# Performance work log

Hardware: AMD Instinct MI355X
Metric: run time of the kernel (lower is better)

## Reference

```python
import jax, jax.numpy as jnp
import numpy as np

H = 256      # hidden_size (hardcoded by view([-1,1,256]) in the torch source)
V = 50257    # output_size / vocab
L = 50       # max_length


def gru_cell(x, h, w_ih, w_hh, b_ih, b_hh):
    """PyTorch GRUCell semantics. x, h: [H]; w_*: [3H, H]; b_*: [3H]."""
    gi = w_ih @ x + b_ih
    gh = w_hh @ h + b_hh
    gi_r, gi_z, gi_n = jnp.split(gi, 3)
    gh_r, gh_z, gh_n = jnp.split(gh, 3)
    r = jax.nn.sigmoid(gi_r + gh_r)
    z = jax.nn.sigmoid(gi_z + gh_z)
    n = jnp.tanh(gi_n + r * gh_n)
    return (1.0 - z) * n + z * h


def setup_inputs() -> dict:
    key = jax.random.key(0)
    ks = jax.random.split(key, 24)
    p = lambda k, shape: (0.02 * jax.random.normal(k, shape)).astype(jnp.float32)
    d = {}
    d["token"] = jax.random.randint(ks[0], (1,), 0, V)
    d["hidden"] = jax.random.normal(ks[1], (1, 1, H), dtype=jnp.float32)
    d["encoder_outputs"] = jax.random.normal(ks[2], (L, H), dtype=jnp.float32)
    d["emb"] = p(ks[3], (V, H))
    d["attn_W"] = p(ks[4], (L, 2 * H)); d["attn_b"] = jnp.zeros((L,), jnp.float32)
    d["comb_W"] = p(ks[5], (H, 2 * H)); d["comb_b"] = jnp.zeros((H,), jnp.float32)
    # bidirectional GRU: forward (f) and reverse (b) direction weights
    d["w_ih_f"] = p(ks[6], (3 * H, H)); d["w_hh_f"] = p(ks[7], (3 * H, H))
    d["b_ih_f"] = jnp.zeros((3 * H,), jnp.float32); d["b_hh_f"] = jnp.zeros((3 * H,), jnp.float32)
    d["w_ih_b"] = p(ks[8], (3 * H, H)); d["w_hh_b"] = p(ks[9], (3 * H, H))
    d["b_ih_b"] = jnp.zeros((3 * H,), jnp.float32); d["b_hh_b"] = jnp.zeros((3 * H,), jnp.float32)
    # second (unidirectional) GRU
    d["w_ih_g"] = p(ks[10], (3 * H, H)); d["w_hh_g"] = p(ks[11], (3 * H, H))
    d["b_ih_g"] = jnp.zeros((3 * H,), jnp.float32); d["b_hh_g"] = jnp.zeros((3 * H,), jnp.float32)
    d["out_W"] = p(ks[12], (V, H)); d["out_b"] = jnp.zeros((V,), jnp.float32)
    return d


def reference(token, hidden, encoder_outputs, emb, attn_W, attn_b, comb_W, comb_b,
              w_ih_f, w_hh_f, b_ih_f, b_hh_f, w_ih_b, w_hh_b, b_ih_b, b_hh_b,
              w_ih_g, w_hh_g, b_ih_g, b_hh_g, out_W, out_b):
    # dropout is treated as identity (eval mode)
    e = emb[token[0]]                       # [H] embedded token
    h0 = hidden[0, 0]                       # [H]
    # attention weights over encoder positions
    aw = jax.nn.softmax(jax.nn.relu(attn_W @ jnp.concatenate([e, h0]) + attn_b))  # [L]
    applied = aw @ encoder_outputs          # [H]
    x = jax.nn.relu(comb_W @ jnp.concatenate([e, applied]) + comb_b)              # [H]
    # bidirectional GRU, seq_len=1: both directions see the same step, init hidden = h0
    hf = gru_cell(x, h0, w_ih_f, w_hh_f, b_ih_f, b_hh_f)
    hb = gru_cell(x, h0, w_ih_b, w_hh_b, b_ih_b, b_hh_b)
    hm = 0.5 * (hf + hb)                    # torch.mean(bihidden, dim=0)
    # bioutput (1,1,512) viewed as (2,1,256) -> second GRU runs 2 steps
    h1 = gru_cell(hf, hm, w_ih_g, w_hh_g, b_ih_g, b_hh_g)
    h2 = gru_cell(hb, h1, w_ih_g, w_hh_g, b_ih_g, b_hh_g)
    logp = jax.nn.log_softmax(out_W @ h1 + out_b)  # output[0] = first timestep = h1
    return (logp[None, :], h2[None, None, :], aw[None, :])
```

## Files before the change

kernel.cpp:

```cpp
#include <hip/hip_runtime.h>
#include <math.h>

#define H 256
#define L 50
#define V 50257
#define LOGIT_BLKS 786

__device__ __forceinline__ float dot4(float4 a, float4 b) {
    return a.x * b.x + a.y * b.y + a.z * b.z + a.w * b.w;
}

__device__ __forceinline__ float wave_reduce_sum(float v) {
#pragma unroll
    for (int m = 32; m >= 1; m >>= 1) v += __shfl_xor(v, m, 64);
    return v;
}

__device__ __forceinline__ float wave_reduce_max(float v) {
#pragma unroll
    for (int m = 32; m >= 1; m >>= 1) v = fmaxf(v, __shfl_xor(v, m, 64));
    return v;
}

__device__ __forceinline__ float sigmoidf(float x) { return 1.0f / (1.0f + __expf(-x)); }

__device__ __forceinline__ void ms_push(float& m, float& s, float x) {
    float mn = fmaxf(m, x);
    s = s * __expf(m - mn) + __expf(x - mn);
    m = mn;
}
__device__ __forceinline__ void ms_merge(float& m, float& s, float om, float os) {
    float M = fmaxf(m, om);
    float a = (m == -INFINITY) ? 0.f : s * __expf(m - M);
    float c = (om == -INFINITY) ? 0.f : os * __expf(om - M);
    m = M; s = a + c;
}

__device__ __forceinline__ void gru_wave(
    int j, int lane, float4 xv, float4 hv, float hj,
    const float* __restrict__ w_ih, const float* __restrict__ w_hh,
    const float* __restrict__ b_ih, const float* __restrict__ b_hh,
    float* __restrict__ outp)
{
    float gi[3], gh[3];
#pragma unroll
    for (int k = 0; k < 3; ++k) {
        int row = k * H + j;
        const float4* wi4 = (const float4*)(w_ih + (size_t)row * H);
        const float4* wh4 = (const float4*)(w_hh + (size_t)row * H);
        gi[k] = wave_reduce_sum(dot4(wi4[lane], xv)) + b_ih[row];
        gh[k] = wave_reduce_sum(dot4(wh4[lane], hv)) + b_hh[row];
    }
    if (lane == 0) {
        float r = sigmoidf(gi[0] + gh[0]);
        float z = sigmoidf(gi[1] + gh[1]);
        float n = tanhf(gi[2] + r * gh[2]);
        outp[j] = (1.f - z) * n + z * hj;
    }
}

__global__ __launch_bounds__(256) void k_scores(
    const int* __restrict__ token, const float* __restrict__ hidden,
    const float* __restrict__ emb, const float* __restrict__ attn_W,
    const float* __restrict__ attn_b, float* __restrict__ ws_scores)
{
    __shared__ float s_vec[2 * H];
    int t = threadIdx.x, wid = t >> 6, lane = t & 63;
    int tok = token[0];
    s_vec[t] = emb[(size_t)tok * H + t];
    s_vec[H + t] = hidden[t];
    __syncthreads();
    int row = blockIdx.x * 4 + wid;
    if (row < L) {
        float acc = 0.f;
#pragma unroll
        for (int c = 0; c < 8; ++c)
            acc += attn_W[row * 2 * H + c * 64 + lane] * s_vec[c * 64 + lane];
        acc = wave_reduce_sum(acc);
        if (lane == 0) ws_scores[row] = fmaxf(acc + attn_b[row], 0.f);
    }
}

__global__ __launch_bounds__(256) void k_comb(
    const int* __restrict__ token, const float* __restrict__ emb,
    const float* __restrict__ enc, const float* __restrict__ comb_W,
    const float* __restrict__ comb_b, const float* __restrict__ ws_scores,
    float* __restrict__ ws_x, float* __restrict__ out_aw)
{
    __shared__ __align__(16) float s_cat[2 * H];
    __shared__ float s_aw[64];
    int t = threadIdx.x, wid = t >> 6, lane = t & 63;
    int tok = token[0];
    s_cat[t] = emb[(size_t)tok * H + t];
    if (t < 64) {
        float v = (t < L) ? ws_scores[t] : -INFINITY;
        float mx = wave_reduce_max(v);
        float e = (t < L) ? __expf(v - mx) : 0.f;
        float ssum = wave_reduce_sum(e);
        if (t < L) {
            float aw = e / ssum;
            s_aw[t] = aw;
            if (blockIdx.x == 0) out_aw[t] = aw;
        }
    }
    __syncthreads();
    float app = 0.f;
    for (int l = 0; l < L; ++l) app += s_aw[l] * enc[l * H + t];
    s_cat[H + t] = app;
    __syncthreads();
    int row = blockIdx.x * 4 + wid;
    const float4* c4 = (const float4*)s_cat;
    const float4* W4 = (const float4*)(comb_W + (size_t)row * 2 * H);
    float acc = dot4(W4[lane], c4[lane]) + dot4(W4[lane + 64], c4[lane + 64]);
    acc = wave_reduce_sum(acc);
    if (lane == 0) ws_x[row] = fmaxf(acc + comb_b[row], 0.f);
}

__global__ __launch_bounds__(256) void k_gru_fb(
    const float* __restrict__ ws_x, const float* __restrict__ hidden,
    const float* __restrict__ w_ih_f, const float* __restrict__ w_hh_f,
    const float* __restrict__ b_ih_f, const float* __restrict__ b_hh_f,
    const float* __restrict__ w_ih_b, const float* __restrict__ w_hh_b,
    const float* __restrict__ b_ih_b, const float* __restrict__ b_hh_b,
    float* __restrict__ ws_hf, float* __restrict__ ws_hb)
{
    int t = threadIdx.x, wid = t >> 6, lane = t & 63;
    int g = blockIdx.x * 4 + wid;
    int dir = g >> 8, j = g & 255;
    gru_wave(j, lane, ((const float4*)ws_x)[lane], ((const float4*)hidden)[lane],
             hidden[j],
             dir ? w_ih_b : w_ih_f, dir ? w_hh_b : w_hh_f,
             dir ? b_ih_b : b_ih_f, dir ? b_hh_b : b_hh_f,
             dir ? ws_hb : ws_hf);
}

__global__ __launch_bounds__(256) void k_gru(
    const float* __restrict__ xvec, const float* __restrict__ ha,
    const float* __restrict__ hb,
    const float* __restrict__ w_ih, const float* __restrict__ w_hh,
    const float* __restrict__ b_ih, const float* __restrict__ b_hh,
    float* __restrict__ outp)
{
    int t = threadIdx.x, wid = t >> 6, lane = t & 63;
    int j = blockIdx.x * 4 + wid;
    float4 xv = ((const float4*)xvec)[lane];
    float4 hv = ((const float4*)ha)[lane];
    float hj;
    if (hb) {
        float4 bv = ((const float4*)hb)[lane];
        hv = make_float4(0.5f * (hv.x + bv.x), 0.5f * (hv.y + bv.y),
                         0.5f * (hv.z + bv.z), 0.5f * (hv.w + bv.w));
        hj = 0.5f * (ha[j] + hb[j]);
    } else {
        hj = ha[j];
    }
    gru_wave(j, lane, xv, hv, hj, w_ih, w_hh, b_ih, b_hh, outp);
}

__global__ __launch_bounds__(256) void k_logits(
    const float* __restrict__ out_W, const float* __restrict__ out_b,
    const float* __restrict__ h1, float* __restrict__ logits,
    float* __restrict__ part_m, float* __restrict__ part_s)
{
    __shared__ float s_m4[4], s_s4[4];
    int t = threadIdx.x, wid = t >> 6, lane = t & 63;
    float4 hv = ((const float4*)h1)[lane];
    int base = (blockIdx.x * 4 + wid) * 16;
    float m = -INFINITY, s = 0.f;
#pragma unroll 1
    for (int k = 0; k < 16; k += 2) {
        int v = base + k;
        if (v >= V) break;
        const float4* W0 = (const float4*)(out_W + (size_t)v * H);
        float4 a0 = W0[lane];
        bool has2 = (v + 1 < V);
        float4 a1 = has2 ? ((const float4*)(out_W + (size_t)(v + 1) * H))[lane]
                         : make_float4(0.f, 0.f, 0.f, 0.f);
        float x0 = wave_reduce_sum(dot4(a0, hv)) + out_b[v];
        float x1 = wave_reduce_sum(dot4(a1, hv));
        if (lane == 0) logits[v] = x0;
        ms_push(m, s, x0);
        if (has2) {
            x1 += out_b[v + 1];
            if (lane == 0) logits[v + 1] = x1;
            ms_push(m, s, x1);
        }
    }
    if (lane == 0) { s_m4[wid] = m; s_s4[wid] = s; }
    __syncthreads();
    if (t == 0) {
        float M = s_m4[0], S = s_s4[0];
#pragma unroll
        for (int q = 1; q < 4; ++q) ms_merge(M, S, s_m4[q], s_s4[q]);
        part_m[blockIdx.x] = M; part_s[blockIdx.x] = S;
    }
}

__global__ __launch_bounds__(256) void k_final(
    const float* __restrict__ part_m, const float* __restrict__ part_s,
    float* __restrict__ logits)
{
    __shared__ float s_m4[4], s_s4[4];
    __shared__ float s_bcast;
    int t = threadIdx.x, wid = t >> 6, lane = t & 63;
    float m = -INFINITY, s = 0.f;
    for (int idx = t; idx < LOGIT_BLKS; idx += 256)
        ms_merge(m, s, part_m[idx], part_s[idx]);
#pragma unroll
    for (int d = 32; d >= 1; d >>= 1) {
        float om = __shfl_xor(m, d, 64);
        float os = __shfl_xor(s, d, 64);
        ms_merge(m, s, om, os);
    }
    if (lane == 0) { s_m4[wid] = m; s_s4[wid] = s; }
    __syncthreads();
    if (t == 0) {
        float M = s_m4[0], S = s_s4[0];
#pragma unroll
        for (int q = 1; q < 4; ++q) ms_merge(M, S, s_m4[q], s_s4[q]);
        s_bcast = M + logf(S);
    }
    __syncthreads();
    float lse = s_bcast;
    int i = blockIdx.x * 256 + t;
    if (i < V) logits[i] -= lse;
}

extern "C" void kernel_launch(void* const* d_in, const int* in_sizes, int n_in,
                              void* d_out, int out_size, void* d_ws, size_t ws_size,
                              hipStream_t stream)
{
    const int*   token  = (const int*)d_in[0];
    const float* hidden = (const float*)d_in[1];
    const float* enc    = (const float*)d_in[2];
    const float* emb    = (const float*)d_in[3];
    const float* attn_W = (const float*)d_in[4];
    const float* attn_b = (const float*)d_in[5];
    const float* comb_W = (const float*)d_in[6];
    const float* comb_b = (const float*)d_in[7];
    const float* w_ih_f = (const float*)d_in[8];
    const float* w_hh_f = (const float*)d_in[9];
    const float* b_ih_f = (const float*)d_in[10];
    const float* b_hh_f = (const float*)d_in[11];
    const float* w_ih_b = (const float*)d_in[12];
    const float* w_hh_b = (const float*)d_in[13];
    const float* b_ih_b = (const float*)d_in[14];
    const float* b_hh_b = (const float*)d_in[15];
    const float* w_ih_g = (const float*)d_in[16];
    const float* w_hh_g = (const float*)d_in[17];
    const float* b_ih_g = (const float*)d_in[18];
    const float* b_hh_g = (const float*)d_in[19];
    const float* out_W  = (const float*)d_in[20];
    const float* out_b  = (const float*)d_in[21];

    float* out = (float*)d_out;
    float* ws  = (float*)d_ws;
    float* ws_scores = ws;
    float* ws_x      = ws + 64;
    float* ws_hf     = ws + 320;
    float* ws_hb     = ws + 576;
    float* ws_h1     = ws + 832;
    float* part_m    = ws + 1088;
    float* part_s    = ws + 1888;

    k_scores<<<13, 256, 0, stream>>>(token, hidden, emb, attn_W, attn_b, ws_scores);
    k_comb<<<64, 256, 0, stream>>>(token, emb, enc, comb_W, comb_b, ws_scores,
                                   ws_x, out + V + H);
    k_gru_fb<<<128, 256, 0, stream>>>(ws_x, hidden,
                                      w_ih_f, w_hh_f, b_ih_f, b_hh_f,
                                      w_ih_b, w_hh_b, b_ih_b, b_hh_b,
                                      ws_hf, ws_hb);
    k_gru<<<64, 256, 0, stream>>>(ws_hf, ws_hf, ws_hb,
                                  w_ih_g, w_hh_g, b_ih_g, b_hh_g, ws_h1);
    k_gru<<<64, 256, 0, stream>>>(ws_hb, ws_h1, nullptr,
                                  w_ih_g, w_hh_g, b_ih_g, b_hh_g, out + V);
    k_logits<<<LOGIT_BLKS, 256, 0, stream>>>(out_W, out_b, ws_h1, out,
                                             part_m, part_s);
    k_final<<<197, 256, 0, stream>>>(part_m, part_s, out);
}
```

Baseline: 179.0 us.

## Fuse attention scores into comb and second GRU step into logits kernel

Attention score computation moves into k_comb, so every block recomputes the 50 scores redundantly instead of running a separate launch. The second GRU step (h2) no longer gets its own launch; it runs as extra blocks inside the logits kernel, since neither depends on the other. The logits grid shrinks to 512 blocks with 25 rows per wave, which still covers V. Together these remove two kernel launches at the price of redundant attention work in each comb block.

```diff
diff --git a/kernel.cpp b/kernel.cpp
--- a/kernel.cpp
+++ b/kernel.cpp
@@ -4,7 +4,9 @@
 #define H 256
 #define L 50
 #define V 50257
-#define LOGIT_BLKS 786
+#define LOGIT_BLKS 512
+#define ROWS_PER_WAVE 25
+#define GRU2_BLKS 64
 
 __device__ __forceinline__ float dot4(float4 a, float4 b) {
     return a.x * b.x + a.y * b.y + a.z * b.z + a.w * b.w;
@@ -59,32 +61,11 @@
     }
 }
 
-__global__ __launch_bounds__(256) void k_scores(
+__global__ __launch_bounds__(256) void k_comb(
     const int* __restrict__ token, const float* __restrict__ hidden,
     const float* __restrict__ emb, const float* __restrict__ attn_W,
-    const float* __restrict__ attn_b, float* __restrict__ ws_scores)
-{
-    __shared__ float s_vec[2 * H];
-    int t = threadIdx.x, wid = t >> 6, lane = t & 63;
-    int tok = token[0];
-    s_vec[t] = emb[(size_t)tok * H + t];
-    s_vec[H + t] = hidden[t];
-    __syncthreads();
-    int row = blockIdx.x * 4 + wid;
-    if (row < L) {
-        float acc = 0.f;
-#pragma unroll
-        for (int c = 0; c < 8; ++c)
-            acc += attn_W[row * 2 * H + c * 64 + lane] * s_vec[c * 64 + lane];
-        acc = wave_reduce_sum(acc);
-        if (lane == 0) ws_scores[row] = fmaxf(acc + attn_b[row], 0.f);
-    }
-}
-
-__global__ __launch_bounds__(256) void k_comb(
-    const int* __restrict__ token, const float* __restrict__ emb,
-    const float* __restrict__ enc, const float* __restrict__ comb_W,
-    const float* __restrict__ comb_b, const float* __restrict__ ws_scores,
+    const float* __restrict__ attn_b, const float* __restrict__ enc,
+    const float* __restrict__ comb_W, const float* __restrict__ comb_b,
     float* __restrict__ ws_x, float* __restrict__ out_aw)
 {
     __shared__ __align__(16) float s_cat[2 * H];
@@ -92,8 +73,20 @@
     int t = threadIdx.x, wid = t >> 6, lane = t & 63;
     int tok = token[0];
     s_cat[t] = emb[(size_t)tok * H + t];
+    s_cat[H + t] = hidden[t];
+    __syncthreads();
+    const float4* c4 = (const float4*)s_cat;
+    float4 cA = c4[lane];
+    float4 cB = c4[lane + 64];
+    for (int r = wid; r < L; r += 4) {
+        const float4* W4 = (const float4*)(attn_W + (size_t)r * 2 * H);
+        float acc = dot4(W4[lane], cA) + dot4(W4[lane + 64], cB);
+        acc = wave_reduce_sum(acc);
+        if (lane == 0) s_aw[r] = fmaxf(acc + attn_b[r], 0.f);
+    }
+    __syncthreads();
     if (t < 64) {
-        float v = (t < L) ? ws_scores[t] : -INFINITY;
+        float v = (t < L) ? s_aw[t] : -INFINITY;
         float mx = wave_reduce_max(v);
         float e = (t < L) ? __expf(v - mx) : 0.f;
         float ssum = wave_reduce_sum(e);
@@ -109,9 +102,9 @@
     s_cat[H + t] = app;
     __syncthreads();
     int row = blockIdx.x * 4 + wid;
-    const float4* c4 = (const float4*)s_cat;
-    const float4* W4 = (const float4*)(comb_W + (size_t)row * 2 * H);
-    float acc = dot4(W4[lane], c4[lane]) + dot4(W4[lane + 64], c4[lane + 64]);
+    const float4* Wc = (const float4*)(comb_W + (size_t)row * 2 * H);
+    float4 cB2 = c4[lane + 64];
+    float acc = dot4(Wc[lane], cA) + dot4(Wc[lane + 64], cB2);
     acc = wave_reduce_sum(acc);
     if (lane == 0) ws_x[row] = fmaxf(acc + comb_b[row], 0.f);
 }
@@ -159,21 +152,31 @@
 
 __global__ __launch_bounds__(256) void k_logits(
     const float* __restrict__ out_W, const float* __restrict__ out_b,
-    const float* __restrict__ h1, float* __restrict__ logits,
-    float* __restrict__ part_m, float* __restrict__ part_s)
-{
+    const float* __restrict__ h1, const float* __restrict__ hb,
+    const float* __restrict__ w_ih_g, const float* __restrict__ w_hh_g,
+    const float* __restrict__ b_ih_g, const float* __restrict__ b_hh_g,
+    float* __restrict__ out_h2,
+    float* __restrict__ logits, float* __restrict__ part_m,
+    float* __restrict__ part_s)
+{
+    int t = threadIdx.x, wid = t >> 6, lane = t & 63;
+    if (blockIdx.x >= LOGIT_BLKS) {
+        int j = (blockIdx.x - LOGIT_BLKS) * 4 + wid;
+        gru_wave(j, lane, ((const float4*)hb)[lane], ((const float4*)h1)[lane],
+                 h1[j], w_ih_g, w_hh_g, b_ih_g, b_hh_g, out_h2);
+        return;
+    }
     __shared__ float s_m4[4], s_s4[4];
-    int t = threadIdx.x, wid = t >> 6, lane = t & 63;
     float4 hv = ((const float4*)h1)[lane];
-    int base = (blockIdx.x * 4 + wid) * 16;
+    int base = (blockIdx.x * 4 + wid) * ROWS_PER_WAVE;
     float m = -INFINITY, s = 0.f;
 #pragma unroll 1
-    for (int k = 0; k < 16; k += 2) {
+    for (int k = 0; k < ROWS_PER_WAVE; k += 2) {
         int v = base + k;
         if (v >= V) break;
         const float4* W0 = (const float4*)(out_W + (size_t)v * H);
         float4 a0 = W0[lane];
-        bool has2 = (v + 1 < V);
+        bool has2 = (k + 1 < ROWS_PER_WAVE) && (v + 1 < V);
         float4 a1 = has2 ? ((const float4*)(out_W + (size_t)(v + 1) * H))[lane]
                          : make_float4(0.f, 0.f, 0.f, 0.f);
         float x0 = wave_reduce_sum(dot4(a0, hv)) + out_b[v];
@@ -255,26 +258,24 @@
 
     float* out = (float*)d_out;
     float* ws  = (float*)d_ws;
-    float* ws_scores = ws;
-    float* ws_x      = ws + 64;
-    float* ws_hf     = ws + 320;
-    float* ws_hb     = ws + 576;
-    float* ws_h1     = ws + 832;
-    float* part_m    = ws + 1088;
-    float* part_s    = ws + 1888;
-
-    k_scores<<<13, 256, 0, stream>>>(token, hidden, emb, attn_W, attn_b, ws_scores);
-    k_comb<<<64, 256, 0, stream>>>(token, emb, enc, comb_W, comb_b, ws_scores,
-                                   ws_x, out + V + H);
+    float* ws_x      = ws;
+    float* ws_hf     = ws + 256;
+    float* ws_hb     = ws + 512;
+    float* ws_h1     = ws + 768;
+    float* part_m    = ws + 1024;
+    float* part_s    = ws + 1536;
+
+    k_comb<<<64, 256, 0, stream>>>(token, hidden, emb, attn_W, attn_b, enc,
+                                   comb_W, comb_b, ws_x, out + V + H);
     k_gru_fb<<<128, 256, 0, stream>>>(ws_x, hidden,
                                       w_ih_f, w_hh_f, b_ih_f, b_hh_f,
                                       w_ih_b, w_hh_b, b_ih_b, b_hh_b,
                                       ws_hf, ws_hb);
     k_gru<<<64, 256, 0, stream>>>(ws_hf, ws_hf, ws_hb,
                                   w_ih_g, w_hh_g, b_ih_g, b_hh_g, ws_h1);
-    k_gru<<<64, 256, 0, stream>>>(ws_hb, ws_h1, nullptr,
-                                  w_ih_g, w_hh_g, b_ih_g, b_hh_g, out + V);
-    k_logits<<<LOGIT_BLKS, 256, 0, stream>>>(out_W, out_b, ws_h1, out,
-                                             part_m, part_s);
+    k_logits<<<LOGIT_BLKS + GRU2_BLKS, 256, 0, stream>>>(
+        out_W, out_b, ws_h1, ws_hb,
+        w_ih_g, w_hh_g, b_ih_g, b_hh_g, out + V,
+        out, part_m, part_s);
     k_final<<<197, 256, 0, stream>>>(part_m, part_s, out);
 }
```

Result: slower. 186.0 us (+3.9%).
